# Kernel optimization log

Hardware: AMD Instinct MI355X
Metric: run time of the kernel (lower is better)

Reference implementation:

```python
import jax, jax.numpy as jnp
import numpy as np

BATCH = 1024
NUM_CLASSES = 100000
FEAT_DIM = 512


def setup_inputs() -> dict:
    key = jax.random.key(0)
    k1, k2, k3 = jax.random.split(key, 3)
    x = jax.random.normal(k1, (BATCH, FEAT_DIM), dtype=jnp.float32)
    labels = jax.random.randint(k2, (BATCH,), 0, NUM_CLASSES, dtype=jnp.int64)
    # learned parameter: class centers, init as in the torch module (randn * 0.01)
    centers = jax.random.normal(k3, (NUM_CLASSES, FEAT_DIM), dtype=jnp.float32) * 0.01
    return {"x": x, "labels": labels, "centers": centers}


def reference(x, labels, centers):
    # Mathematically identical to: sum over b of ||x[b] - centers[labels[b]]||^2 / batch.
    # The torch code materializes diff [B, C, D] and masks; only the true-label
    # distance per row survives, so gather the target center directly.
    target_centers = centers[labels]                 # [B, D] gather
    diff = x - target_centers                        # [B, D]
    loss = jnp.sum(diff * diff) / x.shape[0]         # scalar
    return loss
```

## Files before the change

kernel.cpp:

```cpp
#include <hip/hip_runtime.h>
#include <hip/hip_bf16.h>


#define BATCH 1024
#define FEAT 512

__global__ __launch_bounds__(128) void cl_row_kernel(
    const float* __restrict__ x,
    const int* __restrict__ labels,
    const float* __restrict__ centers,
    float* __restrict__ partial) {
    const int row = blockIdx.x;
    const int t = threadIdx.x;

    const int lab = labels[row];
    const float4* xr = reinterpret_cast<const float4*>(x + (size_t)row * FEAT);
    const float4* cr = reinterpret_cast<const float4*>(centers + (size_t)lab * FEAT);

    float4 a = xr[t];
    float4 b = cr[t];
    float dx = a.x - b.x;
    float dy = a.y - b.y;
    float dz = a.z - b.z;
    float dw = a.w - b.w;
    float s = dx * dx + dy * dy + dz * dz + dw * dw;

    #pragma unroll
    for (int off = 32; off > 0; off >>= 1)
        s += __shfl_down(s, off, 64);

    __shared__ float wsum[2];
    if ((t & 63) == 0) wsum[t >> 6] = s;
    __syncthreads();
    if (t == 0) partial[row] = wsum[0] + wsum[1];
}

__global__ __launch_bounds__(256) void cl_final_kernel(
    const float* __restrict__ partial,
    float* __restrict__ out) {
    const int t = threadIdx.x;
    float4 v = reinterpret_cast<const float4*>(partial)[t];
    float s = v.x + v.y + v.z + v.w;

    #pragma unroll
    for (int off = 32; off > 0; off >>= 1)
        s += __shfl_down(s, off, 64);

    __shared__ float wsum[4];
    if ((t & 63) == 0) wsum[t >> 6] = s;
    __syncthreads();
    if (t == 0) out[0] = (wsum[0] + wsum[1] + wsum[2] + wsum[3]) * (1.0f / (float)BATCH);
}

extern "C" void kernel_launch(void* const* d_in, const int* in_sizes, int n_in,
                              void* d_out, int out_size, void* d_ws, size_t ws_size,
                              hipStream_t stream) {
    const float* x = (const float*)d_in[0];
    const int* labels = (const int*)d_in[1];
    const float* centers = (const float*)d_in[2];
    float* out = (float*)d_out;
    float* partial = (float*)d_ws;

    cl_row_kernel<<<BATCH, 128, 0, stream>>>(x, labels, centers, partial);
    cl_final_kernel<<<1, 256, 0, stream>>>(partial, out);
}
```

Before: 10.82 us.

## Fuse row and final reductions into one cooperative kernel with grid sync

Replaces the two-kernel launch with a single cooperative kernel of 256 blocks. Each wave handles one row and each block writes a partial sum, then a grid-wide sync lets block 0 reduce the 256 partials. This removes the second kernel launch and its gap, at the cost of the cooperative launch path and grid-barrier overhead. If the cooperative launch fails, it falls back to the old two-kernel path.

```diff
diff --git a/kernel.cpp b/kernel.cpp
--- a/kernel.cpp
+++ b/kernel.cpp
@@ -1,9 +1,62 @@
 #include <hip/hip_runtime.h>
-#include <hip/hip_bf16.h>
+#include <hip/hip_cooperative_groups.h>
+
+namespace cg = cooperative_groups;
 
 
 #define BATCH 1024
 #define FEAT 512
+#define NBLK 256
+#define NTHR 256
+
+__global__ __launch_bounds__(NTHR) void cl_fused(
+    const float* __restrict__ x,
+    const int* __restrict__ labels,
+    const float* __restrict__ centers,
+    float* __restrict__ out,
+    float* __restrict__ partial) {
+    const int b = blockIdx.x;
+    const int t = threadIdx.x;
+    const int wave = t >> 6;
+    const int lane = t & 63;
+    const int row = b * 4 + wave;
+
+    const int lab = labels[row];
+    const float4* xr = reinterpret_cast<const float4*>(x + (size_t)row * FEAT);
+    const float4* cr = reinterpret_cast<const float4*>(centers + (size_t)lab * FEAT);
+
+    float4 a0 = xr[lane];
+    float4 c0 = cr[lane];
+    float4 a1 = xr[lane + 64];
+    float4 c1 = cr[lane + 64];
+
+    float dx0 = a0.x - c0.x, dy0 = a0.y - c0.y, dz0 = a0.z - c0.z, dw0 = a0.w - c0.w;
+    float dx1 = a1.x - c1.x, dy1 = a1.y - c1.y, dz1 = a1.z - c1.z, dw1 = a1.w - c1.w;
+    float s = dx0 * dx0 + dy0 * dy0 + dz0 * dz0 + dw0 * dw0
+            + dx1 * dx1 + dy1 * dy1 + dz1 * dz1 + dw1 * dw1;
+
+    #pragma unroll
+    for (int off = 32; off > 0; off >>= 1)
+        s += __shfl_down(s, off, 64);
+
+    __shared__ float wsum[4];
+    if (lane == 0) wsum[wave] = s;
+    __syncthreads();
+    if (t == 0) partial[b] = wsum[0] + wsum[1] + wsum[2] + wsum[3];
+
+    cg::this_grid().sync();
+
+    if (b == 0) {
+        float v = partial[t];
+        #pragma unroll
+        for (int off = 32; off > 0; off >>= 1)
+            v += __shfl_down(v, off, 64);
+        __shared__ float fsum[4];
+        if (lane == 0) fsum[wave] = v;
+        __syncthreads();
+        if (t == 0) out[0] = (fsum[0] + fsum[1] + fsum[2] + fsum[3]) * (1.0f / (float)BATCH);
+    }
+}
 
 __global__ __launch_bounds__(128) void cl_row_kernel(
     const float* __restrict__ x,
@@ -12,23 +65,16 @@
     float* __restrict__ partial) {
     const int row = blockIdx.x;
     const int t = threadIdx.x;
-
     const int lab = labels[row];
     const float4* xr = reinterpret_cast<const float4*>(x + (size_t)row * FEAT);
     const float4* cr = reinterpret_cast<const float4*>(centers + (size_t)lab * FEAT);
-
     float4 a = xr[t];
-    float4 b = cr[t];
-    float dx = a.x - b.x;
-    float dy = a.y - b.y;
-    float dz = a.z - b.z;
-    float dw = a.w - b.w;
+    float4 c = cr[t];
+    float dx = a.x - c.x, dy = a.y - c.y, dz = a.z - c.z, dw = a.w - c.w;
     float s = dx * dx + dy * dy + dz * dz + dw * dw;
-
     #pragma unroll
     for (int off = 32; off > 0; off >>= 1)
         s += __shfl_down(s, off, 64);
-
     __shared__ float wsum[2];
     if ((t & 63) == 0) wsum[t >> 6] = s;
     __syncthreads();
@@ -41,11 +87,9 @@
     const int t = threadIdx.x;
     float4 v = reinterpret_cast<const float4*>(partial)[t];
     float s = v.x + v.y + v.z + v.w;
-
     #pragma unroll
     for (int off = 32; off > 0; off >>= 1)
         s += __shfl_down(s, off, 64);
-
     __shared__ float wsum[4];
     if ((t & 63) == 0) wsum[t >> 6] = s;
     __syncthreads();
@@ -61,6 +105,12 @@
     float* out = (float*)d_out;
     float* partial = (float*)d_ws;
 
-    cl_row_kernel<<<BATCH, 128, 0, stream>>>(x, labels, centers, partial);
-    cl_final_kernel<<<1, 256, 0, stream>>>(partial, out);
+    void* args[] = {(void*)&x, (void*)&labels, (void*)&centers, (void*)&out, (void*)&partial};
+    hipError_t err = hipLaunchCooperativeKernel((const void*)cl_fused,
+                                                dim3(NBLK), dim3(NTHR),
+                                                args, 0, stream);
+    if (err != hipSuccess) {
+        cl_row_kernel<<<BATCH, 128, 0, stream>>>(x, labels, centers, partial);
+        cl_final_kernel<<<1, 256, 0, stream>>>(partial, out);
+    }
 }
```

Measured after the change: 41.27 us. +281.6%, slower.

## Fuse row and final reduction into one kernel with flag-based handoff

Applied to the files above, without the earlier changes.

Merges the per-row kernel and the final reduction into a single launch. Each block now handles four rows (one per wave, two float4 loads per lane), publishes its block sum with a release-stored magic flag, and block 0 spins on the flags to gather and reduce the partials. This removes the second kernel launch and the dependency gap between kernels. In exchange block 0 must busy-wait on the other blocks, which assumes they get scheduled, and it relies on the flags starting out different from the magic value and being reset after each call.

```diff
diff --git a/kernel.cpp b/kernel.cpp
--- a/kernel.cpp
+++ b/kernel.cpp
@@ -1,55 +1,75 @@
 #include <hip/hip_runtime.h>
-#include <hip/hip_bf16.h>
 
 
 #define BATCH 1024
 #define FEAT 512
+#define NBLK 256
+#define NTHR 256
+#define MAGIC 0x13572468u
 
-__global__ __launch_bounds__(128) void cl_row_kernel(
+__global__ __launch_bounds__(NTHR) void cl_fused_flags(
     const float* __restrict__ x,
     const int* __restrict__ labels,
     const float* __restrict__ centers,
-    float* __restrict__ partial) {
-    const int row = blockIdx.x;
+    float* __restrict__ out,
+    float* __restrict__ partial,
+    unsigned int* __restrict__ flags) {
+    const int b = blockIdx.x;
     const int t = threadIdx.x;
+    const int wave = t >> 6;
+    const int lane = t & 63;
+    const int row = b * 4 + wave;
 
     const int lab = labels[row];
     const float4* xr = reinterpret_cast<const float4*>(x + (size_t)row * FEAT);
     const float4* cr = reinterpret_cast<const float4*>(centers + (size_t)lab * FEAT);
 
-    float4 a = xr[t];
-    float4 b = cr[t];
-    float dx = a.x - b.x;
-    float dy = a.y - b.y;
-    float dz = a.z - b.z;
-    float dw = a.w - b.w;
-    float s = dx * dx + dy * dy + dz * dz + dw * dw;
+    float4 a0 = xr[lane];
+    float4 c0 = cr[lane];
+    float4 a1 = xr[lane + 64];
+    float4 c1 = cr[lane + 64];
 
-    #pragma unroll
-    for (int off = 32; off > 0; off >>= 1)
-        s += __shfl_down(s, off, 64);
-
-    __shared__ float wsum[2];
-    if ((t & 63) == 0) wsum[t >> 6] = s;
-    __syncthreads();
-    if (t == 0) partial[row] = wsum[0] + wsum[1];
-}
-
-__global__ __launch_bounds__(256) void cl_final_kernel(
-    const float* __restrict__ partial,
-    float* __restrict__ out) {
-    const int t = threadIdx.x;
-    float4 v = reinterpret_cast<const float4*>(partial)[t];
-    float s = v.x + v.y + v.z + v.w;
+    float dx0 = a0.x - c0.x, dy0 = a0.y - c0.y, dz0 = a0.z - c0.z, dw0 = a0.w - c0.w;
+    float dx1 = a1.x - c1.x, dy1 = a1.y - c1.y, dz1 = a1.z - c1.z, dw1 = a1.w - c1.w;
+    float s = dx0 * dx0 + dy0 * dy0 + dz0 * dz0 + dw0 * dw0
+            + dx1 * dx1 + dy1 * dy1 + dz1 * dz1 + dw1 * dw1;
 
     #pragma unroll
     for (int off = 32; off > 0; off >>= 1)
         s += __shfl_down(s, off, 64);
 
     __shared__ float wsum[4];
-    if ((t & 63) == 0) wsum[t >> 6] = s;
+    if (lane == 0) wsum[wave] = s;
     __syncthreads();
-    if (t == 0) out[0] = (wsum[0] + wsum[1] + wsum[2] + wsum[3]) * (1.0f / (float)BATCH);
+    const float blocksum = wsum[0] + wsum[1] + wsum[2] + wsum[3];
+
+    if (b != 0) {
+        if (t == 0) {
+            __hip_atomic_store(&partial[b], blocksum, __ATOMIC_RELAXED, __HIP_MEMORY_SCOPE_AGENT);
+            __hip_atomic_store(&flags[b], MAGIC, __ATOMIC_RELEASE, __HIP_MEMORY_SCOPE_AGENT);
+        }
+        return;
+    }
+
+    float v;
+    if (t == 0) {
+        v = blocksum;
+    } else {
+        while (__hip_atomic_load(&flags[t], __ATOMIC_ACQUIRE, __HIP_MEMORY_SCOPE_AGENT) != MAGIC) {
+        }
+        v = __hip_atomic_load(&partial[t], __ATOMIC_RELAXED, __HIP_MEMORY_SCOPE_AGENT);
+        __hip_atomic_store(&flags[t], 0u, __ATOMIC_RELAXED, __HIP_MEMORY_SCOPE_AGENT);
+    }
+
+    #pragma unroll
+    for (int off = 32; off > 0; off >>= 1)
+        v += __shfl_down(v, off, 64);
+
+    __shared__ float fsum[4];
+    if (lane == 0) fsum[wave] = v;
+    __syncthreads();
+    if (t == 0)
+        out[0] = (fsum[0] + fsum[1] + fsum[2] + fsum[3]) * (1.0f / (float)BATCH);
 }
 
 extern "C" void kernel_launch(void* const* d_in, const int* in_sizes, int n_in,
@@ -60,7 +80,7 @@
     const float* centers = (const float*)d_in[2];
     float* out = (float*)d_out;
     float* partial = (float*)d_ws;
+    unsigned int* flags = (unsigned int*)(partial + NBLK);
 
-    cl_row_kernel<<<BATCH, 128, 0, stream>>>(x, labels, centers, partial);
-    cl_final_kernel<<<1, 256, 0, stream>>>(partial, out);
+    cl_fused_flags<<<NBLK, NTHR, 0, stream>>>(x, labels, centers, out, partial, flags);
 }
```

Result: slower. 12.10 us (+11.9%).
